# Kernel tuning notes

Measured on AMD Instinct MI355X. Metric: run time of the kernel, lower is better.

## Reference

```python
import jax, jax.numpy as jnp
import numpy as np

B, S, D, H, E, K = 2, 1024, 1024, 512, 16, 4  # batch, seq, hidden, expert inter, n_experts, top_k
HS = 2 * H  # shared expert inter dim = num_shared_experts * moe_inter_dim


def silu(z):
    return z * jax.nn.sigmoid(z)


def setup_inputs() -> dict:
    key = jax.random.key(0)
    ks = jax.random.split(key, 8)
    sc = lambda fan_in: 1.0 / np.sqrt(fan_in)
    x = jax.random.normal(ks[0], (B, S, D), jnp.float32)
    gate_w = jax.random.normal(ks[1], (E, D), jnp.float32) * sc(D)
    ws_in = jax.random.normal(ks[2], (D, HS), jnp.float32) * sc(D)
    vs_in = jax.random.normal(ks[3], (D, HS), jnp.float32) * sc(D)
    ws_out = jax.random.normal(ks[4], (HS, D), jnp.float32) * sc(HS)
    e_win = jax.random.normal(ks[5], (E, D, H), jnp.float32) * sc(D)
    e_vin = jax.random.normal(ks[6], (E, D, H), jnp.float32) * sc(D)
    e_wout = jax.random.normal(ks[7], (E, H, D), jnp.float32) * sc(H)
    return {"x": x, "gate_w": gate_w, "ws_in": ws_in, "vs_in": vs_in,
            "ws_out": ws_out, "e_win": e_win, "e_vin": e_vin, "e_wout": e_wout}


def reference(x, gate_w, ws_in, vs_in, ws_out, e_win, e_vin, e_wout):
    b, s, d = x.shape
    T = b * s
    xf = x.reshape(T, d)

    # --- Gate (eval path: biases buffer is zero / unused) ---
    g = jax.nn.sigmoid(xf @ gate_w.T)                      # [T, E]
    topv, topi = jax.lax.top_k(g, K)                        # [T, K]
    wn = topv / jnp.sum(topv, axis=-1, keepdims=True)       # normalized top-k weights
    # sparse combine matrix [T, E]: zero for unrouted experts -> exact same math
    # as the original per-expert masked gather/scatter loop
    combine = jnp.zeros_like(g).at[jnp.arange(T)[:, None], topi].add(wn)

    # --- Routed experts (SwiGLU), batched over experts ---
    hin = jnp.einsum('td,edh->eth', xf, e_win)              # [E, T, H]
    vin = jnp.einsum('td,edh->eth', xf, e_vin)              # [E, T, H]
    h = silu(hin) * vin * combine.T[:, :, None]             # weight before down-proj
    routed = jnp.einsum('eth,ehd->td', h, e_wout)           # [T, D]

    # --- Shared expert (SwiGLU with inter = num_shared * moe_inter) ---
    shared = (silu(xf @ ws_in) * (xf @ vs_in)) @ ws_out     # [T, D]

    return (shared + routed).reshape(b, s, d)
```

## Files before the change

kernel.cpp:

```cpp
#include <hip/hip_runtime.h>
#include <hip/hip_bf16.h>
#include <math.h>

typedef __attribute__((ext_vector_type(4))) float f32x4;
typedef __attribute__((ext_vector_type(8))) short s16x8;
typedef __hip_bfloat16 bf16;

constexpr int TOK = 2048;
constexpr int DIM = 1024;
constexpr int HID = 512;
constexpr int NE  = 16;
constexpr int NK  = 4;
constexpr int NHS = 1024;
constexpr int NPAIR = TOK * NK;

constexpr int UP_GRID = 128 + 4 * 80;
constexpr int DN_GRID = 64 + 4 * 80;

#define MFMA(a, b, c) __builtin_amdgcn_mfma_f32_16x16x32_bf16(a, b, c, 0, 0, 0)

#define GLOAD_LDS(gp, lp)                                                        \
  __builtin_amdgcn_global_load_lds(                                              \
      (const __attribute__((address_space(1))) unsigned int*)(gp),               \
      (__attribute__((address_space(3))) unsigned int*)(lp), 16, 0, 0)

template <int CH>
static __device__ __forceinline__ void stage_p(const bf16* const* rp, int k0,
                                               bf16* lds, int tid) {
  int wid = tid >> 6;
#pragma unroll
  for (int i = 0; i < CH; ++i) {
    int c = i * 512 + tid;
    int row = c >> 3;
    int slot = c & 7;
    int j = slot ^ (row & 7);
    const bf16* g = rp[i] + k0 + j * 8;
    bf16* l = lds + (size_t)(i * 512 + wid * 64) * 8;
    GLOAD_LDS(g, l);
  }
}

static __device__ __forceinline__ s16x8 frag(const bf16* lds, int row, int kc) {
  return *(const s16x8*)(lds + row * 64 + ((kc ^ (row & 7)) << 3));
}

static __device__ __forceinline__ float b2f(short u) {
  union { unsigned int i; float f; } c;
  c.i = ((unsigned int)(unsigned short)u) << 16;
  return c.f;
}

struct bf16x4 { bf16 a, b, c, d; };
struct alignas(16) bf16x8 { bf16 v[8]; };


static __device__ __forceinline__ void tr64(const float* __restrict__ src,
                                            bf16* __restrict__ dst, int R, int C,
                                            int bx, int by, float (*t)[65], int tid) {
  int r0 = by * 64, c0 = bx * 64;
#pragma unroll
  for (int i = 0; i < 4; ++i) {
    int row = i * 16 + (tid >> 4);
    int col = (tid & 15) * 4;
    float4 v = *(const float4*)(src + (size_t)(r0 + row) * C + c0 + col);
    t[row][col] = v.x; t[row][col + 1] = v.y;
    t[row][col + 2] = v.z; t[row][col + 3] = v.w;
  }
  __syncthreads();
  int c = tid >> 2;
  int rb = (tid & 3) * 16;
  bf16x8 o0, o1;
#pragma unroll
  for (int k = 0; k < 8; ++k) o0.v[k] = __float2bfloat16(t[rb + k][c]);
#pragma unroll
  for (int k = 0; k < 8; ++k) o1.v[k] = __float2bfloat16(t[rb + 8 + k][c]);
  bf16* d = dst + (size_t)(c0 + c) * R + r0 + rb;
  *(bf16x8*)d = o0;
  *(bf16x8*)(d + 8) = o1;
}

__global__ __launch_bounds__(256) void prep1(const float* __restrict__ ws_in,
                                             const float* __restrict__ vs_in,
                                             const float* __restrict__ e_win,
                                             const float* __restrict__ e_vin,
                                             bf16* __restrict__ wsinT, bf16* __restrict__ vsinT,
                                             bf16* __restrict__ ewinT, bf16* __restrict__ evinT) {
  __shared__ float t[64][65];
  int bid = blockIdx.x, tid = threadIdx.x;
  if (bid < 256) {
    tr64(ws_in, wsinT, DIM, NHS, bid & 15, bid >> 4, t, tid);
  } else if (bid < 512) {
    int b = bid - 256;
    tr64(vs_in, vsinT, DIM, NHS, b & 15, b >> 4, t, tid);
  } else if (bid < 2560) {
    int b = bid - 512, e = b >> 7; b &= 127;
    tr64(e_win + (size_t)e * DIM * HID, ewinT + (size_t)e * DIM * HID,
         DIM, HID, b & 7, b >> 3, t, tid);
  } else {
    int b = bid - 2560, e = b >> 7; b &= 127;
    tr64(e_vin + (size_t)e * DIM * HID, evinT + (size_t)e * DIM * HID,
         DIM, HID, b & 7, b >> 3, t, tid);
  }
}

__global__ __launch_bounds__(256) void prep2(const float* __restrict__ ws_out,
                                             const float* __restrict__ e_wout,
                                             bf16* __restrict__ wsoutT,
                                             bf16* __restrict__ ewoutT) {
  __shared__ float t[64][65];
  int bid = blockIdx.x, tid = threadIdx.x;
  if (bid < 256) {
    tr64(ws_out, wsoutT, NHS, DIM, bid & 15, bid >> 4, t, tid);
  } else {
    int b = bid - 256, e = b >> 7; b &= 127;
    tr64(e_wout + (size_t)e * HID * DIM, ewoutT + (size_t)e * HID * DIM,
         HID, DIM, b & 15, b >> 4, t, tid);
  }
}


__global__ __launch_bounds__(256) void gate_scores(const float* __restrict__ x,
                                                   const float* __restrict__ gw,
                                                   bf16* __restrict__ xb,
                                                   float* __restrict__ scores) {
  int lane = threadIdx.x & 63, wid = threadIdx.x >> 6;
  int t = blockIdx.x * 4 + wid;
  const float* xr = x + (size_t)t * DIM + lane * 16;
  float4 x4[4];
#pragma unroll
  for (int q = 0; q < 4; ++q) x4[q] = *(const float4*)(xr + q * 4);
  {
    bf16* xo = xb + (size_t)t * DIM + lane * 16;
#pragma unroll
    for (int q = 0; q < 4; ++q) {
      bf16x4 o{__float2bfloat16(x4[q].x), __float2bfloat16(x4[q].y),
               __float2bfloat16(x4[q].z), __float2bfloat16(x4[q].w)};
      *reinterpret_cast<bf16x4*>(xo + q * 4) = o;
    }
  }
  float s[NE];
#pragma unroll
  for (int e = 0; e < NE; ++e) {
    const float* wr_ = gw + (size_t)e * DIM + lane * 16;
    float a = 0.f;
#pragma unroll
    for (int q = 0; q < 4; ++q) {
      float4 w4 = *(const float4*)(wr_ + q * 4);
      a += x4[q].x * w4.x + x4[q].y * w4.y + x4[q].z * w4.z + x4[q].w * w4.w;
    }
    s[e] = a;
  }
#pragma unroll
  for (int e = 0; e < NE; ++e)
#pragma unroll
    for (int off = 32; off; off >>= 1) s[e] += __shfl_xor(s[e], off);
  if (lane == 0) {
#pragma unroll
    for (int e = 0; e < NE; ++e) scores[(size_t)t * NE + e] = s[e];
  }
}

__global__ __launch_bounds__(256) void topk_hist(const float* __restrict__ scores,
                                                 int* __restrict__ topi,
                                                 float* __restrict__ topw,
                                                 int* __restrict__ counts) {
  __shared__ int h[NE];
  int tid = threadIdx.x;
  int t = blockIdx.x * 256 + tid;
  if (tid < NE) h[tid] = 0;
  __syncthreads();
  float g[NE];
  const float* sr = scores + (size_t)t * NE;
#pragma unroll
  for (int q = 0; q < 4; ++q) {
    float4 v = *(const float4*)(sr + q * 4);
    g[q * 4 + 0] = 1.f / (1.f + expf(-v.x));
    g[q * 4 + 1] = 1.f / (1.f + expf(-v.y));
    g[q * 4 + 2] = 1.f / (1.f + expf(-v.z));
    g[q * 4 + 3] = 1.f / (1.f + expf(-v.w));
  }
  unsigned used = 0;
  int bi[NK]; float bv[NK];
  float sum = 0.f;
#pragma unroll
  for (int j = 0; j < NK; ++j) {
    int best = 0; float v = -1e30f;
#pragma unroll
    for (int e = 0; e < NE; ++e)
      if (!((used >> e) & 1u) && g[e] > v) { v = g[e]; best = e; }
    used |= 1u << best; bi[j] = best; bv[j] = v; sum += v;
  }
  float inv = 1.f / sum;
#pragma unroll
  for (int j = 0; j < NK; ++j) {
    topi[t * NK + j] = bi[j];
    topw[t * NK + j] = bv[j] * inv;
    atomicAdd(&h[bi[j]], 1);
  }
  __syncthreads();
  if (tid < NE) atomicAdd(&counts[tid], h[tid]);
}

__global__ __launch_bounds__(64) void route_small(const int* __restrict__ counts,
                                                  int* __restrict__ offs,
                                                  int* __restrict__ segs,
                                                  int* __restrict__ nseg,
                                                  int* __restrict__ cursor) {
  if (threadIdx.x != 0) return;
  int o = 0;
#pragma unroll
  for (int e = 0; e < NE; ++e) { offs[e] = o; cursor[e * 32] = 0; o += counts[e]; }
  int s = 0;
  for (int e = 0; e < NE; ++e)
    for (int m = 0; m < counts[e]; m += 128) segs[s++] = (e << 16) | m;
  nseg[0] = s;
}

__global__ __launch_bounds__(256) void scatter_pairs(const int* __restrict__ topi,
                                                     const float* __restrict__ topw,
                                                     const int* __restrict__ offs,
                                                     int* __restrict__ cursor,
                                                     int* __restrict__ tok_list,
                                                     float* __restrict__ w_list,
                                                     int* __restrict__ pair_slot) {
  int p = blockIdx.x * 256 + threadIdx.x;
  if (p >= NPAIR) return;
  int e = topi[p];
  int rank = atomicAdd(&cursor[e * 32], 1);
  int slot = offs[e] + rank;
  tok_list[slot] = p >> 2;
  w_list[slot] = topw[p];
  pair_slot[p] = slot;
}


__global__ __launch_bounds__(512, 4) void up_all(
    const bf16* __restrict__ xb, const bf16* __restrict__ wsinT,
    const bf16* __restrict__ vsinT, const bf16* __restrict__ ewinT,
    const bf16* __restrict__ evinT, const int* __restrict__ tok_list,
    const float* __restrict__ w_list, const int* __restrict__ counts,
    const int* __restrict__ offs, const int* __restrict__ segs,
    const int* __restrict__ nseg, bf16* __restrict__ hsb,
    bf16* __restrict__ hre) {
  int bid = blockIdx.x;
  int j = (bid & 7) * (UP_GRID / 8) + (bid >> 3);
  int nj = 128 + 4 * nseg[0];
  if (j >= nj) return;
  int tid = threadIdx.x, lane = tid & 63, wid = tid >> 6;
  int wr = wid >> 2, wc = wid & 3;

  bool is_shared = (j < 128);
  int m0, n0, cnt = TOK, off_e = 0;
  const bf16 *w1, *w2;
  if (is_shared) {
    m0 = (j >> 3) * 128; n0 = j & 7;
    w1 = wsinT; w2 = vsinT;
  } else {
    int r = j - 128;
    int sv = segs[r >> 2]; n0 = r & 3;
    int e = sv >> 16; m0 = sv & 0xffff;
    cnt = counts[e]; off_e = offs[e];
    w1 = ewinT + (size_t)e * HID * DIM;
    w2 = evinT + (size_t)e * HID * DIM;
  }

  const bf16* ap[2]; const bf16* bp[4];
#pragma unroll
  for (int i = 0; i < 2; ++i) {
    int row = (i * 512 + tid) >> 3;
    int gr = is_shared ? (m0 + row) : tok_list[off_e + min(m0 + row, cnt - 1)];
    ap[i] = xb + (size_t)gr * DIM;
  }
#pragma unroll
  for (int i = 0; i < 4; ++i) {
    int r = (i * 512 + tid) >> 3;
    int ridx = n0 * 128 + (r >> 5) * 16 + (r & 15);
    bp[i] = ((r & 16) ? w2 : w1) + (size_t)ridx * DIM;
  }

  __shared__ alignas(16) bf16 As[128 * 64], Bs[256 * 64];
  f32x4 acc[4][4];
  f32x4 z4 = {0.f, 0.f, 0.f, 0.f};
#pragma unroll
  for (int m = 0; m < 4; ++m)
#pragma unroll
    for (int q = 0; q < 4; ++q) acc[m][q] = z4;

  for (int k0 = 0; k0 < DIM; k0 += 64) {
    __syncthreads();
    stage_p<2>(ap, k0, As, tid);
    stage_p<4>(bp, k0, Bs, tid);
    __syncthreads();
#pragma unroll
    for (int ks = 0; ks < 2; ++ks) {
      int r16 = lane & 15, kc = (ks << 2) + (lane >> 4);
      s16x8 a[4];
#pragma unroll
      for (int m = 0; m < 4; ++m) a[m] = frag(As, wr * 64 + m * 16 + r16, kc);
#pragma unroll
      for (int q = 0; q < 4; ++q) {
        s16x8 b = frag(Bs, wc * 64 + q * 16 + r16, kc);
#pragma unroll
        for (int m = 0; m < 4; ++m) acc[m][q] = MFMA(a[m], b, acc[m][q]);
      }
    }
  }
#pragma unroll
  for (int m = 0; m < 4; ++m)
#pragma unroll
    for (int q = 0; q < 4; q += 2) {
      int c = n0 * 128 + (wc * 2 + (q >> 1)) * 16 + (lane & 15);
#pragma unroll
      for (int i = 0; i < 4; ++i) {
        int r = wr * 64 + m * 16 + (lane >> 4) * 4 + i;
        float z = acc[m][q][i], v = acc[m][q + 1][i];
        float h = z / (1.f + __expf(-z)) * v;
        if (is_shared) {
          hsb[(size_t)(m0 + r) * NHS + c] = __float2bfloat16(h);
        } else {
          int gr = m0 + r;
          if (gr < cnt)
            hre[(size_t)(off_e + gr) * HID + c] =
                __float2bfloat16(h * w_list[off_e + gr]);
        }
      }
    }
}


__global__ __launch_bounds__(512, 4) void down_all(
    const bf16* __restrict__ hsb, const bf16* __restrict__ wsoutT,
    const bf16* __restrict__ hre, const bf16* __restrict__ ewoutT,
    const int* __restrict__ tok_list, const int* __restrict__ counts,
    const int* __restrict__ offs, const int* __restrict__ segs,
    const int* __restrict__ nseg, float* __restrict__ out,
    bf16* __restrict__ hrd) {
  int bid = blockIdx.x;
  int j = (bid & 7) * (DN_GRID / 8) + (bid >> 3);
  int nj = 64 + 4 * nseg[0];
  if (j >= nj) return;
  int tid = threadIdx.x, lane = tid & 63, wid = tid >> 6;
  int wr = wid >> 2, wc = wid & 3;

  bool is_shared = (j < 64);
  int m0, n0, cnt = TOK, off_e = 0, K, ldA, ldB;
  const bf16 *Abase, *Bbase;
  if (is_shared) {
    m0 = (j >> 2) * 128; n0 = j & 3;
    Abase = hsb; ldA = NHS; K = NHS;
    Bbase = wsoutT; ldB = NHS;
  } else {
    int r = j - 64;
    int sv = segs[r >> 2]; n0 = r & 3;
    int e = sv >> 16; m0 = sv & 0xffff;
    cnt = counts[e]; off_e = offs[e];
    Abase = hre + (size_t)off_e * HID; ldA = HID; K = HID;
    Bbase = ewoutT + (size_t)e * DIM * HID; ldB = HID;
  }

  const bf16* ap[2]; const bf16* bp[4];
#pragma unroll
  for (int i = 0; i < 2; ++i) {
    int row = (i * 512 + tid) >> 3;
    int gr = is_shared ? (m0 + row) : min(m0 + row, cnt - 1);
    ap[i] = Abase + (size_t)gr * ldA;
  }
#pragma unroll
  for (int i = 0; i < 4; ++i) {
    int r = (i * 512 + tid) >> 3;
    bp[i] = Bbase + (size_t)(n0 * 256 + r) * ldB;
  }

  __shared__ alignas(16) bf16 As[128 * 64], Bs[256 * 64];
  f32x4 acc[4][4];
  f32x4 z4 = {0.f, 0.f, 0.f, 0.f};
#pragma unroll
  for (int m = 0; m < 4; ++m)
#pragma unroll
    for (int q = 0; q < 4; ++q) acc[m][q] = z4;

  int NT = K / 64;
  for (int kt = 0; kt < NT; ++kt) {
    int k0 = kt * 64;
    __syncthreads();
    stage_p<2>(ap, k0, As, tid);
    stage_p<4>(bp, k0, Bs, tid);
    __syncthreads();
#pragma unroll
    for (int ks = 0; ks < 2; ++ks) {
      int r16 = lane & 15, kc = (ks << 2) + (lane >> 4);
      s16x8 a[4];
#pragma unroll
      for (int m = 0; m < 4; ++m) a[m] = frag(As, wr * 64 + m * 16 + r16, kc);
#pragma unroll
      for (int q = 0; q < 4; ++q) {
        s16x8 b = frag(Bs, wc * 64 + q * 16 + r16, kc);
#pragma unroll
        for (int m = 0; m < 4; ++m) acc[m][q] = MFMA(a[m], b, acc[m][q]);
      }
    }
  }
#pragma unroll
  for (int m = 0; m < 4; ++m)
#pragma unroll
    for (int q = 0; q < 4; ++q) {
      int c = n0 * 256 + wc * 64 + q * 16 + (lane & 15);
#pragma unroll
      for (int i = 0; i < 4; ++i) {
        int r = wr * 64 + m * 16 + (lane >> 4) * 4 + i;
        if (is_shared) {
          out[(size_t)(m0 + r) * DIM + c] = acc[m][q][i];
        } else {
          int gr = m0 + r;
          if (gr < cnt)
            hrd[(size_t)(off_e + gr) * DIM + c] = __float2bfloat16(acc[m][q][i]);
        }
      }
    }
}


__global__ __launch_bounds__(256) void finish_add(const bf16* __restrict__ hrd,
                                                  const int* __restrict__ pair_slot,
                                                  float* __restrict__ out) {
  int idx = blockIdx.x * 256 + threadIdx.x;
  int t = idx >> 7;
  int c0 = (idx & 127) * 8;
  int4 s4 = *(const int4*)(pair_slot + t * 4);
  float acc[8];
  float* o = out + (size_t)t * DIM + c0;
#pragma unroll
  for (int k = 0; k < 8; ++k) acc[k] = o[k];
  int sl[4] = {s4.x, s4.y, s4.z, s4.w};
#pragma unroll
  for (int j = 0; j < 4; ++j) {
    s16x8 v = *(const s16x8*)(hrd + (size_t)sl[j] * DIM + c0);
#pragma unroll
    for (int k = 0; k < 8; ++k) acc[k] += b2f(v[k]);
  }
#pragma unroll
  for (int k = 0; k < 8; ++k) o[k] = acc[k];
}


extern "C" void kernel_launch(void* const* d_in, const int* in_sizes, int n_in,
                              void* d_out, int out_size, void* d_ws, size_t ws_size,
                              hipStream_t stream) {
  const float* x      = (const float*)d_in[0];
  const float* gw     = (const float*)d_in[1];
  const float* ws_in  = (const float*)d_in[2];
  const float* vs_in  = (const float*)d_in[3];
  const float* ws_out = (const float*)d_in[4];
  const float* e_win  = (const float*)d_in[5];
  const float* e_vin  = (const float*)d_in[6];
  const float* e_wout = (const float*)d_in[7];
  float* out = (float*)d_out;

  char* p = (char*)d_ws;
  bf16* xb     = (bf16*)p;  p += (size_t)TOK * DIM * 2;
  bf16* wsinT  = (bf16*)p;
  bf16* wsoutT = wsinT;
  p += (size_t)NHS * DIM * 2;
  bf16* vsinT  = (bf16*)p;  p += (size_t)NHS * DIM * 2;
  bf16* hsb    = (bf16*)p;  p += (size_t)TOK * NHS * 2;
  bf16* ewinT  = (bf16*)p;
  bf16* ewoutT = ewinT;
  p += (size_t)NE * DIM * HID * 2;
  bf16* evinT  = (bf16*)p;
  bf16* hrd    = evinT;
  p += (size_t)NE * DIM * HID * 2;
  bf16* hre    = (bf16*)p;  p += (size_t)(NPAIR + 128) * HID * 2;
  int*   topi      = (int*)p;    p += (size_t)NPAIR * 4;
  float* topw      = (float*)p;  p += (size_t)NPAIR * 4;
  int*   tok_list  = (int*)p;    p += (size_t)NPAIR * 4;
  float* w_list    = (float*)p;  p += (size_t)NPAIR * 4;
  int*   pair_slot = (int*)p;    p += (size_t)NPAIR * 4;
  float* scores    = (float*)p;  p += (size_t)TOK * NE * 4;
  int*   counts    = (int*)p;    p += 64;
  int*   offs      = (int*)p;    p += 64;
  int*   cursor    = (int*)p;    p += NE * 32 * 4;
  int*   segs      = (int*)p;    p += 128 * 4;
  int*   nseg      = (int*)p;    p += 64;

  hipMemsetAsync(counts, 0, NE * sizeof(int), stream);
  gate_scores<<<TOK / 4, 256, 0, stream>>>(x, gw, xb, scores);
  topk_hist<<<TOK / 256, 256, 0, stream>>>(scores, topi, topw, counts);
  route_small<<<1, 64, 0, stream>>>(counts, offs, segs, nseg, cursor);
  scatter_pairs<<<NPAIR / 256, 256, 0, stream>>>(topi, topw, offs, cursor,
                                                 tok_list, w_list, pair_slot);

  prep1<<<4608, 256, 0, stream>>>(ws_in, vs_in, e_win, e_vin,
                                  wsinT, vsinT, ewinT, evinT);

  up_all<<<UP_GRID, 512, 0, stream>>>(xb, wsinT, vsinT, ewinT, evinT, tok_list,
                                      w_list, counts, offs, segs, nseg, hsb, hre);

  prep2<<<2304, 256, 0, stream>>>(ws_out, e_wout, wsoutT, ewoutT);

  down_all<<<DN_GRID, 512, 0, stream>>>(hsb, wsoutT, hre, ewoutT, tok_list,
                                        counts, offs, segs, nseg, out, hrd);
  finish_add<<<TOK * DIM / 8 / 256, 256, 0, stream>>>(hrd, pair_slot, out);
}
```

Before: 155.0 us.

## Double-buffer B tiles and prefetch next K-slice in up/down MoE GEMMs

Both grouped GEMM kernels now double-buffer the weight (B) tile in LDS. The next B slice is issued with global_load_lds before computing the current one, and the A tile is refilled after a second barrier. Manual vmcnt waits, raw s_barrier and setprio replace the two __syncthreads per iteration, so global loads can overlap the MFMA work. The cost is extra LDS per block, which may lower occupancy, and the hand-counted vmcnt(4) depends on exactly how many loads stage_p issues.

Measured after the change: 146.7 us. 5.4% less time.

```diff
diff --git a/kernel.cpp b/kernel.cpp
--- a/kernel.cpp
+++ b/kernel.cpp
@@ -278,7 +278,7 @@
     bp[i] = ((r & 16) ? w2 : w1) + (size_t)ridx * DIM;
   }
 
-  __shared__ alignas(16) bf16 As[128 * 64], Bs[256 * 64];
+  __shared__ alignas(16) bf16 As[128 * 64], Bs[2][256 * 64];
   f32x4 acc[4][4];
   f32x4 z4 = {0.f, 0.f, 0.f, 0.f};
 #pragma unroll
@@ -286,11 +286,22 @@
 #pragma unroll
     for (int q = 0; q < 4; ++q) acc[m][q] = z4;
 
-  for (int k0 = 0; k0 < DIM; k0 += 64) {
-    __syncthreads();
-    stage_p<2>(ap, k0, As, tid);
-    stage_p<4>(bp, k0, Bs, tid);
-    __syncthreads();
+  constexpr int NT = DIM / 64;
+  stage_p<2>(ap, 0, As, tid);
+  stage_p<4>(bp, 0, Bs[0], tid);
+
+  for (int kt = 0; kt < NT; ++kt) {
+    if (kt + 1 < NT) {
+      stage_p<4>(bp, (kt + 1) * 64, Bs[(kt + 1) & 1], tid);
+      asm volatile("s_waitcnt vmcnt(4)" ::: "memory");
+    } else {
+      asm volatile("s_waitcnt vmcnt(0)" ::: "memory");
+    }
+    __builtin_amdgcn_sched_barrier(0);
+    __builtin_amdgcn_s_barrier();
+    __builtin_amdgcn_sched_barrier(0);
+    const bf16* Bc = Bs[kt & 1];
+    __builtin_amdgcn_s_setprio(1);
 #pragma unroll
     for (int ks = 0; ks < 2; ++ks) {
       int r16 = lane & 15, kc = (ks << 2) + (lane >> 4);
@@ -299,11 +310,16 @@
       for (int m = 0; m < 4; ++m) a[m] = frag(As, wr * 64 + m * 16 + r16, kc);
 #pragma unroll
       for (int q = 0; q < 4; ++q) {
-        s16x8 b = frag(Bs, wc * 64 + q * 16 + r16, kc);
+        s16x8 b = frag(Bc, wc * 64 + q * 16 + r16, kc);
 #pragma unroll
         for (int m = 0; m < 4; ++m) acc[m][q] = MFMA(a[m], b, acc[m][q]);
       }
     }
+    __builtin_amdgcn_s_setprio(0);
+    __builtin_amdgcn_sched_barrier(0);
+    __builtin_amdgcn_s_barrier();
+    __builtin_amdgcn_sched_barrier(0);
+    if (kt + 1 < NT) stage_p<2>(ap, (kt + 1) * 64, As, tid);
   }
 #pragma unroll
   for (int m = 0; m < 4; ++m)
@@ -371,7 +387,7 @@
     bp[i] = Bbase + (size_t)(n0 * 256 + r) * ldB;
   }
 
-  __shared__ alignas(16) bf16 As[128 * 64], Bs[256 * 64];
+  __shared__ alignas(16) bf16 As[128 * 64], Bs[2][256 * 64];
   f32x4 acc[4][4];
   f32x4 z4 = {0.f, 0.f, 0.f, 0.f};
 #pragma unroll
@@ -380,12 +396,21 @@
     for (int q = 0; q < 4; ++q) acc[m][q] = z4;
 
   int NT = K / 64;
+  stage_p<2>(ap, 0, As, tid);
+  stage_p<4>(bp, 0, Bs[0], tid);
+
   for (int kt = 0; kt < NT; ++kt) {
-    int k0 = kt * 64;
-    __syncthreads();
-    stage_p<2>(ap, k0, As, tid);
-    stage_p<4>(bp, k0, Bs, tid);
-    __syncthreads();
+    if (kt + 1 < NT) {
+      stage_p<4>(bp, (kt + 1) * 64, Bs[(kt + 1) & 1], tid);
+      asm volatile("s_waitcnt vmcnt(4)" ::: "memory");
+    } else {
+      asm volatile("s_waitcnt vmcnt(0)" ::: "memory");
+    }
+    __builtin_amdgcn_sched_barrier(0);
+    __builtin_amdgcn_s_barrier();
+    __builtin_amdgcn_sched_barrier(0);
+    const bf16* Bc = Bs[kt & 1];
+    __builtin_amdgcn_s_setprio(1);
 #pragma unroll
     for (int ks = 0; ks < 2; ++ks) {
       int r16 = lane & 15, kc = (ks << 2) + (lane >> 4);
@@ -394,11 +419,16 @@
       for (int m = 0; m < 4; ++m) a[m] = frag(As, wr * 64 + m * 16 + r16, kc);
 #pragma unroll
       for (int q = 0; q < 4; ++q) {
-        s16x8 b = frag(Bs, wc * 64 + q * 16 + r16, kc);
+        s16x8 b = frag(Bc, wc * 64 + q * 16 + r16, kc);
 #pragma unroll
         for (int m = 0; m < 4; ++m) acc[m][q] = MFMA(a[m], b, acc[m][q]);
       }
     }
+    __builtin_amdgcn_s_setprio(0);
+    __builtin_amdgcn_sched_barrier(0);
+    __builtin_amdgcn_s_barrier();
+    __builtin_amdgcn_sched_barrier(0);
+    if (kt + 1 < NT) stage_p<2>(ap, (kt + 1) * 64, As, tid);
   }
 #pragma unroll
   for (int m = 0; m < 4; ++m)
```
